# Kernel optimization log

Hardware: AMD Instinct MI355X
Metric: run time of the kernel (lower is better)

## Reference

```python
import jax, jax.numpy as jnp
import numpy as np

EPS = 1e-9

def _cheb_attention_conv(X_real, X_imag, lap_real, lap_imag,
                         Wa_real, Wa_imag, ba_real, ba_imag,
                         modrelu_b, W_real, W_imag):
    B, N, C = X_real.shape
    # --- attention scores: CVLinear over cat([x_i, x_j]) == (X@W1)_i + (X@W2)_j + b ---
    W1r, W2r = Wa_real[:C, 0], Wa_real[C:, 0]  # [C]
    W1i, W2i = Wa_imag[:C, 0], Wa_imag[C:, 0]
    # complex matvec: (Xr + iXi)(Wr + iWi)
    si_r = X_real @ W1r - X_imag @ W1i          # [B,N] contribution of x_i
    si_i = X_real @ W1i + X_imag @ W1r
    sj_r = X_real @ W2r - X_imag @ W2i          # [B,N] contribution of x_j
    sj_i = X_real @ W2i + X_imag @ W2r
    sc_r = si_r[:, :, None] + sj_r[:, None, :] + ba_real[0]   # [B,N,N]
    sc_i = si_i[:, :, None] + sj_i[:, None, :] + ba_imag[0]
    # --- learnable modReLU: relu(|z| + b) * z/|z| ---
    mag = jnp.sqrt(sc_r * sc_r + sc_i * sc_i)
    scale = jax.nn.relu(mag + modrelu_b[0]) / (mag + EPS)
    sc_r = sc_r * scale
    sc_i = sc_i * scale
    # --- split complex softmax over last dim ---
    a_r = jax.nn.softmax(sc_r, axis=-1)
    a_i = jax.nn.softmax(sc_i, axis=-1)
    # --- reweight Laplacian polynomials (complex mult, broadcast over k) ---
    L_r = lap_real * a_r[:, None] - lap_imag * a_i[:, None]   # [B,K+1,N,N]
    L_i = lap_real * a_i[:, None] + lap_imag * a_r[:, None]
    # --- sum_k (L_k X) W_k, complex ---
    LX_r = jnp.einsum('bkij,bjc->bkic', L_r, X_real) - jnp.einsum('bkij,bjc->bkic', L_i, X_imag)
    LX_i = jnp.einsum('bkij,bjc->bkic', L_r, X_imag) + jnp.einsum('bkij,bjc->bkic', L_i, X_real)
    out_r = jnp.einsum('bkic,kco->bio', LX_r, W_real) - jnp.einsum('bkic,kco->bio', LX_i, W_imag)
    out_i = jnp.einsum('bkic,kco->bio', LX_r, W_imag) + jnp.einsum('bkic,kco->bio', LX_i, W_real)
    return out_r, out_i


def setup_inputs() -> dict:
    key = jax.random.key(0)
    ks = jax.random.split(key, 8)
    B, N, C, CO, K1 = 48, 512, 64, 64, 5
    # weights normalized to unit complex magnitude like the torch init
    wr = jax.random.uniform(ks[4], (K1, C, CO), minval=-1.0, maxval=1.0) / np.sqrt(CO)
    wi = jax.random.uniform(ks[5], (K1, C, CO), minval=-1.0, maxval=1.0) / np.sqrt(CO)
    m = jnp.sqrt(wr * wr + wi * wi)
    return {
        'X_real': jax.random.normal(ks[0], (B, N, C), jnp.float32),
        'X_imag': jax.random.normal(ks[1], (B, N, C), jnp.float32),
        'lap_real': jax.random.normal(ks[2], (B, K1, N, N), jnp.float32) * 0.1,
        'lap_imag': jax.random.normal(ks[3], (B, K1, N, N), jnp.float32) * 0.1,
        'Wa_real': jax.random.normal(ks[6], (2 * C, 1), jnp.float32) * 0.1,
        'Wa_imag': jax.random.normal(ks[7], (2 * C, 1), jnp.float32) * 0.1,
        'ba_real': jnp.zeros((1,), jnp.float32),
        'ba_imag': jnp.zeros((1,), jnp.float32),
        'modrelu_b': jnp.zeros((1,), jnp.float32),
        'W_real': (wr / m).astype(jnp.float32),
        'W_imag': (wi / m).astype(jnp.float32),
    }


def reference(X_real, X_imag, lap_real, lap_imag, Wa_real, Wa_imag,
              ba_real, ba_imag, modrelu_b, W_real, W_imag):
    out_r, out_i = _cheb_attention_conv(X_real, X_imag, lap_real, lap_imag,
                                        Wa_real, Wa_imag, ba_real, ba_imag,
                                        modrelu_b, W_real, W_imag)
    return out_r, out_i
```

## Files before the change

kernel.cpp:

```cpp
#include <hip/hip_runtime.h>

#define EPSF 1e-9f

typedef __attribute__((ext_vector_type(8))) short short8;
typedef __attribute__((ext_vector_type(4))) float f32x4;
typedef __attribute__((ext_vector_type(4))) unsigned int u32x4;
typedef __attribute__((ext_vector_type(2))) unsigned int u32x2;

__device__ __forceinline__ unsigned pkbf(float lo, float hi) {
  unsigned r;
  asm("v_cvt_pk_bf16_f32 %0, %1, %2" : "=v"(r) : "v"(lo), "v"(hi));
  return r;
}
__device__ __forceinline__ short8 mk8(unsigned a, unsigned b, unsigned c, unsigned d) {
  u32x4 u = {a, b, c, d};
  return __builtin_bit_cast(short8, u);
}

__global__ __launch_bounds__(256) void k_s(
    const float* __restrict__ Xr, const float* __restrict__ Xi,
    const float* __restrict__ War, const float* __restrict__ Wai,
    float4* __restrict__ s4, float2* __restrict__ sj2)
{
  int t = threadIdx.x;
  int nf = blockIdx.x * 32 + (t >> 3);
  int c0 = (t & 7) * 8;
  const f32x4* xr = (const f32x4*)(Xr + (size_t)nf * 64 + c0);
  const f32x4* xi = (const f32x4*)(Xi + (size_t)nf * 64 + c0);
  const f32x4* w1r = (const f32x4*)(War + c0);
  const f32x4* w2r = (const f32x4*)(War + 64 + c0);
  const f32x4* w1i = (const f32x4*)(Wai + c0);
  const f32x4* w2i = (const f32x4*)(Wai + 64 + c0);
  float sir = 0.f, sii = 0.f, sjr = 0.f, sji = 0.f;
#pragma unroll
  for (int h = 0; h < 2; ++h) {
    f32x4 a = xr[h], bb = xi[h];
    f32x4 u1r = w1r[h], u1i = w1i[h], u2r = w2r[h], u2i = w2i[h];
#pragma unroll
    for (int e = 0; e < 4; ++e) {
      sir += a[e] * u1r[e] - bb[e] * u1i[e];
      sii += a[e] * u1i[e] + bb[e] * u1r[e];
      sjr += a[e] * u2r[e] - bb[e] * u2i[e];
      sji += a[e] * u2i[e] + bb[e] * u2r[e];
    }
  }
#pragma unroll
  for (int off = 1; off < 8; off <<= 1) {
    sir += __shfl_xor(sir, off);
    sii += __shfl_xor(sii, off);
    sjr += __shfl_xor(sjr, off);
    sji += __shfl_xor(sji, off);
  }
  if ((t & 7) == 0) {
    s4[nf] = make_float4(sir, sii, sjr, sji);
    sj2[nf] = make_float2(sjr, sji);
  }
}

__global__ __launch_bounds__(256) void k_stats(
    const float4* __restrict__ s4, const float2* __restrict__ sj2,
    const float* __restrict__ bar, const float* __restrict__ bai,
    const float* __restrict__ modbp, float4* __restrict__ stats)
{
  __shared__ float2 sh[512];
  int t = threadIdx.x;
  int b = blockIdx.x >> 4;
  int i0 = (blockIdx.x & 15) * 32;
  sh[t] = sj2[(size_t)b * 512 + t];
  sh[t + 256] = sj2[(size_t)b * 512 + t + 256];
  __syncthreads();
  float ba_r = bar[0], ba_i = bai[0], modb = modbp[0];
  int i = i0 + (t >> 3), jl = t & 7;
  float4 sv = s4[(size_t)b * 512 + i];
  float sirb = sv.x + ba_r, siib = sv.y + ba_i;
  float mr = -1e30f, mi = -1e30f;
  for (int jj = 0; jj < 64; ++jj) {
    float2 sj = sh[jl * 64 + jj];
    float scr = sirb + sj.x, sci = siib + sj.y;
    float mag = sqrtf(scr * scr + sci * sci);
    float sc = fmaxf(mag + modb, 0.f) * __builtin_amdgcn_rcpf(mag + EPSF);
    mr = fmaxf(mr, scr * sc);
    mi = fmaxf(mi, sci * sc);
  }
#pragma unroll
  for (int off = 1; off < 8; off <<= 1) {
    mr = fmaxf(mr, __shfl_xor(mr, off));
    mi = fmaxf(mi, __shfl_xor(mi, off));
  }
  float er = 0.f, ei = 0.f;
  for (int jj = 0; jj < 64; ++jj) {
    float2 sj = sh[jl * 64 + jj];
    float scr = sirb + sj.x, sci = siib + sj.y;
    float mag = sqrtf(scr * scr + sci * sci);
    float sc = fmaxf(mag + modb, 0.f) * __builtin_amdgcn_rcpf(mag + EPSF);
    er += __expf(scr * sc - mr);
    ei += __expf(sci * sc - mi);
  }
#pragma unroll
  for (int off = 1; off < 8; off <<= 1) {
    er += __shfl_xor(er, off);
    ei += __shfl_xor(ei, off);
  }
  if (jl == 0)
    stats[(size_t)b * 512 + i] = make_float4(mr, 1.f / er, mi, 1.f / ei);
}

__global__ __launch_bounds__(256) void k_y(
    const float* __restrict__ Xr, const float* __restrict__ Xi,
    const float* __restrict__ Wr, const float* __restrict__ Wi,
    u32x4* __restrict__ yfrag)
{
  __shared__ __align__(16) short WtR[64 * 72];
  __shared__ __align__(16) short WtI[64 * 72];
  __shared__ __align__(16) short Yt[4][2][64 * 24];
  int bk = blockIdx.x;
  int b = bk / 5, k = bk % 5;
  int t = threadIdx.x;
  {
    int o = t & 63, cbase = (t >> 6) * 16;
    const float* wr = Wr + (size_t)k * 4096;
    const float* wi = Wi + (size_t)k * 4096;
#pragma unroll
    for (int cc = 0; cc < 16; cc += 2) {
      int c = cbase + cc;
      *(unsigned*)&WtR[o * 72 + c] = pkbf(wr[c * 64 + o], wr[(c + 1) * 64 + o]);
      *(unsigned*)&WtI[o * 72 + c] = pkbf(wi[c * 64 + o], wi[(c + 1) * 64 + o]);
    }
  }
  __syncthreads();
  int w = t >> 6, l = t & 63;
  int lane15 = l & 15, quad = l >> 4;
  short* ytR = &Yt[w][0][0];
  short* ytI = &Yt[w][1][0];
  for (int qq = 0; qq < 8; ++qq) {
    int q = w * 8 + qq;
    int j = q * 16 + lane15;
    const f32x4* pxr = (const f32x4*)(Xr + ((size_t)b * 512 + j) * 64 + quad * 8);
    const f32x4* pxi = (const f32x4*)(Xi + ((size_t)b * 512 + j) * 64 + quad * 8);
    f32x4 xr0 = pxr[0], xr1 = pxr[1], xr8 = pxr[8], xr9 = pxr[9];
    f32x4 xi0 = pxi[0], xi1 = pxi[1], xi8 = pxi[8], xi9 = pxi[9];
    short8 axr[2], axi[2];
    axr[0] = mk8(pkbf(xr0[0], xr0[1]), pkbf(xr0[2], xr0[3]), pkbf(xr1[0], xr1[1]), pkbf(xr1[2], xr1[3]));
    axr[1] = mk8(pkbf(xr8[0], xr8[1]), pkbf(xr8[2], xr8[3]), pkbf(xr9[0], xr9[1]), pkbf(xr9[2], xr9[3]));
    axi[0] = mk8(pkbf(xi0[0], xi0[1]), pkbf(xi0[2], xi0[3]), pkbf(xi1[0], xi1[1]), pkbf(xi1[2], xi1[3]));
    axi[1] = mk8(pkbf(xi8[0], xi8[1]), pkbf(xi8[2], xi8[3]), pkbf(xi9[0], xi9[1]), pkbf(xi9[2], xi9[3]));
    f32x4 aR1[4], aR2[4], aI[4];
#pragma unroll
    for (int os = 0; os < 4; ++os) {
      aR1[os] = f32x4{0.f, 0.f, 0.f, 0.f};
      aR2[os] = f32x4{0.f, 0.f, 0.f, 0.f};
      aI[os] = f32x4{0.f, 0.f, 0.f, 0.f};
    }
#pragma unroll
    for (int kc = 0; kc < 2; ++kc) {
#pragma unroll
      for (int os = 0; os < 4; ++os) {
        int widx = (os * 16 + lane15) * 72 + kc * 32 + quad * 8;
        short8 wrF = *(const short8*)&WtR[widx];
        short8 wiF = *(const short8*)&WtI[widx];
        aR1[os] = __builtin_amdgcn_mfma_f32_16x16x32_bf16(axr[kc], wrF, aR1[os], 0, 0, 0);
        aR2[os] = __builtin_amdgcn_mfma_f32_16x16x32_bf16(axi[kc], wiF, aR2[os], 0, 0, 0);
        aI[os]  = __builtin_amdgcn_mfma_f32_16x16x32_bf16(axr[kc], wiF, aI[os], 0, 0, 0);
        aI[os]  = __builtin_amdgcn_mfma_f32_16x16x32_bf16(axi[kc], wrF, aI[os], 0, 0, 0);
      }
    }
#pragma unroll
    for (int os = 0; os < 4; ++os) {
      f32x4 R = aR1[os] - aR2[os];
      f32x4 I = aI[os];
      int ya = (os * 16 + lane15) * 24 + quad * 4;
      *(u32x2*)&ytR[ya] = u32x2{pkbf(R[0], R[1]), pkbf(R[2], R[3])};
      *(u32x2*)&ytI[ya] = u32x2{pkbf(I[0], I[1]), pkbf(I[2], I[3])};
    }
#pragma unroll
    for (int part = 0; part < 2; ++part) {
      const short* yt = part ? ytI : ytR;
#pragma unroll
      for (int h = 0; h < 2; ++h) {
        short8 unit = *(const short8*)&yt[l * 24 + h * 8];
        size_t line = (((size_t)(b * 5 + k) * 2 + part) * 16 + (q >> 1)) * 4 + (l >> 4);
        size_t idx = line * 64 + ((q & 1) * 2 + h) * 16 + (l & 15);
        yfrag[idx] = __builtin_bit_cast(u32x4, unit);
      }
    }
  }
}

__global__ __launch_bounds__(256) __attribute__((amdgpu_waves_per_eu(2, 2)))
void k_main(
    const float* __restrict__ lapr, const float* __restrict__ lapi,
    const float4* __restrict__ s4, const float4* __restrict__ stats,
    const float2* __restrict__ sj2, const u32x4* __restrict__ yfrag,
    const float* __restrict__ bar, const float* __restrict__ bai,
    const float* __restrict__ modbp,
    float* __restrict__ out_r, float* __restrict__ out_i)
{
  __shared__ __align__(16) f32x4 red[2][64][8];

  const int g = blockIdx.x;
  const int b = (g & 7) + ((g >> 8) << 3);
  const int it = (g >> 3) & 31;
  const int t = threadIdx.x;
  const int w = t >> 6;
  const int l = t & 63;
  const int lane15 = l & 15, quad = l >> 4;
  const int gi = it * 16 + lane15;

  float ba_r = bar[0], ba_i = bai[0], modb = modbp[0];
  float4 sv = s4[(size_t)b * 512 + gi];
  float4 st = stats[(size_t)b * 512 + gi];
  float sirb = sv.x + ba_r, siib = sv.y + ba_i;
  float maxr = st.x, rsr = st.y, maxi = st.z, rsi = st.w;

  f32x4 accR[4], accI[4];
#pragma unroll
  for (int os = 0; os < 4; ++os) {
    accR[os] = f32x4{0.f, 0.f, 0.f, 0.f};
    accI[os] = f32x4{0.f, 0.f, 0.f, 0.f};
  }

  const size_t NN = (size_t)512 * 512;
  const float* lapr_b = lapr + ((size_t)b * 5 * 512 + gi) * 512;
  const float* lapi_b = lapi + ((size_t)b * 5 * 512 + gi) * 512;
  const u32x4* yb = yfrag + (size_t)b * 5 * 8192 + l;

  for (int jsw = 0; jsw < 4; ++jsw) {
    const int js = w * 4 + jsw;
    const int jq = js * 32 + quad * 8;

    const f32x4* sjp = (const f32x4*)(sj2 + (size_t)b * 512 + jq);
    f32x4 sjv0 = sjp[0], sjv1 = sjp[1], sjv2 = sjp[2], sjv3 = sjp[3];

    f32x4 LR[5][2], LI[5][2];
#pragma unroll
    for (int k = 0; k < 5; ++k) {
      const f32x4* pr = (const f32x4*)(lapr_b + (size_t)k * NN + jq);
      const f32x4* pi_ = (const f32x4*)(lapi_b + (size_t)k * NN + jq);
      LR[k][0] = __builtin_nontemporal_load(pr);
      LR[k][1] = __builtin_nontemporal_load(pr + 1);
      LI[k][0] = __builtin_nontemporal_load(pi_);
      LI[k][1] = __builtin_nontemporal_load(pi_ + 1);
    }
    __builtin_amdgcn_sched_barrier(0);

    float sjr[8] = {sjv0[0], sjv0[2], sjv1[0], sjv1[2], sjv2[0], sjv2[2], sjv3[0], sjv3[2]};
    float sjimag[8] = {sjv0[1], sjv0[3], sjv1[1], sjv1[3], sjv2[1], sjv2[3], sjv3[1], sjv3[3]};
    float ar[8], ai[8];
#pragma unroll
    for (int e = 0; e < 8; ++e) {
      float scr = sirb + sjr[e];
      float sci = siib + sjimag[e];
      float mag = __builtin_amdgcn_sqrtf(fmaf(scr, scr, sci * sci));
      float sc = fmaxf(mag + modb, 0.f) * __builtin_amdgcn_rcpf(mag + EPSF);
      ar[e] = __expf(fmaf(scr, sc, -maxr)) * rsr;
      ai[e] = __expf(fmaf(sci, sc, -maxi)) * rsi;
    }

#pragma unroll
    for (int k = 0; k < 5; ++k) {
      float lrv[8], liv[8];
#pragma unroll
      for (int e = 0; e < 4; ++e) {
        lrv[e]     = LR[k][0][e] * ar[e]     - LI[k][0][e] * ai[e];
        liv[e]     = LR[k][0][e] * ai[e]     + LI[k][0][e] * ar[e];
        lrv[4 + e] = LR[k][1][e] * ar[4 + e] - LI[k][1][e] * ai[4 + e];
        liv[4 + e] = LR[k][1][e] * ai[4 + e] + LI[k][1][e] * ar[4 + e];
      }
      unsigned p0 = pkbf(lrv[0], lrv[1]), p1 = pkbf(lrv[2], lrv[3]);
      unsigned p2 = pkbf(lrv[4], lrv[5]), p3 = pkbf(lrv[6], lrv[7]);
      unsigned q0 = pkbf(liv[0], liv[1]), q1 = pkbf(liv[2], liv[3]);
      unsigned q2 = pkbf(liv[4], liv[5]), q3 = pkbf(liv[6], liv[7]);
      short8 Ar = mk8(p0, p1, p2, p3);
      short8 Ai = mk8(q0, q1, q2, q3);
      short8 An = mk8(q0 ^ 0x80008000u, q1 ^ 0x80008000u,
                      q2 ^ 0x80008000u, q3 ^ 0x80008000u);

      const u32x4* yk = yb + (size_t)k * 8192 + (size_t)(js * 4) * 64;
#pragma unroll
      for (int os = 0; os < 4; ++os) {
        short8 br8 = __builtin_bit_cast(short8, yk[os * 64]);
        short8 bi8 = __builtin_bit_cast(short8, yk[4096 + os * 64]);
        accR[os] = __builtin_amdgcn_mfma_f32_16x16x32_bf16(Ar, br8, accR[os], 0, 0, 0);
        accR[os] = __builtin_amdgcn_mfma_f32_16x16x32_bf16(An, bi8, accR[os], 0, 0, 0);
        accI[os] = __builtin_amdgcn_mfma_f32_16x16x32_bf16(Ar, bi8, accI[os], 0, 0, 0);
        accI[os] = __builtin_amdgcn_mfma_f32_16x16x32_bf16(Ai, br8, accI[os], 0, 0, 0);
      }
    }
  }

  if (w >= 2) {
#pragma unroll
    for (int os = 0; os < 4; ++os) {
      red[w - 2][l][os] = accR[os];
      red[w - 2][l][4 + os] = accI[os];
    }
  }
  __syncthreads();
  if (w < 2) {
#pragma unroll
    for (int os = 0; os < 4; ++os) {
      accR[os] += red[w][l][os];
      accI[os] += red[w][l][4 + os];
    }
  }
  __syncthreads();
  if (w == 1) {
#pragma unroll
    for (int os = 0; os < 4; ++os) {
      red[0][l][os] = accR[os];
      red[0][l][4 + os] = accI[os];
    }
  }
  __syncthreads();
  if (w == 0) {
#pragma unroll
    for (int os = 0; os < 4; ++os) {
      accR[os] += red[0][l][os];
      accI[os] += red[0][l][4 + os];
      int oc = os * 16 + lane15;
#pragma unroll
      for (int r = 0; r < 4; ++r) {
        size_t oidx = ((size_t)b * 512 + it * 16 + quad * 4 + r) * 64 + oc;
        out_r[oidx] = accR[os][r];
        out_i[oidx] = accI[os][r];
      }
    }
  }
}

extern "C" void kernel_launch(void* const* d_in, const int* in_sizes, int n_in,
                              void* d_out, int out_size, void* d_ws, size_t ws_size,
                              hipStream_t stream) {
  const float* Xr = (const float*)d_in[0];
  const float* Xi = (const float*)d_in[1];
  const float* lapr = (const float*)d_in[2];
  const float* lapi = (const float*)d_in[3];
  const float* War = (const float*)d_in[4];
  const float* Wai = (const float*)d_in[5];
  const float* bar = (const float*)d_in[6];
  const float* bai = (const float*)d_in[7];
  const float* modb = (const float*)d_in[8];
  const float* Wr = (const float*)d_in[9];
  const float* Wi = (const float*)d_in[10];

  char* wsb = (char*)d_ws;
  float4* s4 = (float4*)wsb;
  float4* stats = (float4*)(wsb + 393216);
  float2* sj2 = (float2*)(wsb + 786432);
  u32x4* yfrag = (u32x4*)(wsb + 983040);

  float* out_r = (float*)d_out;
  float* out_i = out_r + (size_t)48 * 512 * 64;

  k_s<<<768, 256, 0, stream>>>(Xr, Xi, War, Wai, s4, sj2);
  k_stats<<<768, 256, 0, stream>>>(s4, sj2, bar, bai, modb, stats);
  k_y<<<240, 256, 0, stream>>>(Xr, Xi, Wr, Wi, yfrag);
  k_main<<<1536, 256, 0, stream>>>(lapr, lapi, s4, stats, sj2, yfrag,
                                   bar, bai, modb, out_r, out_i);
}
```

Measured before the change: 190.8 us.

## Split k_main into single-wave blocks with partial outputs and separate reduction kernel

```diff
diff --git a/kernel.cpp b/kernel.cpp
--- a/kernel.cpp
+++ b/kernel.cpp
@@ -113,7 +113,8 @@
   __shared__ __align__(16) short WtR[64 * 72];
   __shared__ __align__(16) short WtI[64 * 72];
   __shared__ __align__(16) short Yt[4][2][64 * 24];
-  int bk = blockIdx.x;
+  int bk = blockIdx.x >> 2;
+  int jh = blockIdx.x & 3;
   int b = bk / 5, k = bk % 5;
   int t = threadIdx.x;
   {
@@ -132,8 +133,8 @@
   int lane15 = l & 15, quad = l >> 4;
   short* ytR = &Yt[w][0][0];
   short* ytI = &Yt[w][1][0];
-  for (int qq = 0; qq < 8; ++qq) {
-    int q = w * 8 + qq;
+  for (int qq = 0; qq < 2; ++qq) {
+    int q = jh * 8 + w * 2 + qq;
     int j = q * 16 + lane15;
     const f32x4* pxr = (const f32x4*)(Xr + ((size_t)b * 512 + j) * 64 + quad * 8);
     const f32x4* pxi = (const f32x4*)(Xi + ((size_t)b * 512 + j) * 64 + quad * 8);
@@ -186,23 +187,23 @@
   }
 }
 
-__global__ __launch_bounds__(256) __attribute__((amdgpu_waves_per_eu(2, 2)))
+__global__ __launch_bounds__(64) __attribute__((amdgpu_waves_per_eu(4, 4)))
 void k_main(
     const float* __restrict__ lapr, const float* __restrict__ lapi,
     const float4* __restrict__ s4, const float4* __restrict__ stats,
     const float2* __restrict__ sj2, const u32x4* __restrict__ yfrag,
     const float* __restrict__ bar, const float* __restrict__ bai,
     const float* __restrict__ modbp,
-    float* __restrict__ out_r, float* __restrict__ out_i)
-{
-  __shared__ __align__(16) f32x4 red[2][64][8];
-
+    float* __restrict__ partR, float* __restrict__ partI)
+{
   const int g = blockIdx.x;
-  const int b = (g & 7) + ((g >> 8) << 3);
-  const int it = (g >> 3) & 31;
-  const int t = threadIdx.x;
-  const int w = t >> 6;
-  const int l = t & 63;
+  const int bl = g & 7;
+  const int g2 = g >> 3;
+  const int it = g2 & 31;
+  const int sl = (g2 >> 5) & 3;
+  const int bh = g2 >> 7;
+  const int b = bl + (bh << 3);
+  const int l = threadIdx.x;
   const int lane15 = l & 15, quad = l >> 4;
   const int gi = it * 16 + lane15;
 
@@ -225,7 +226,7 @@
   const u32x4* yb = yfrag + (size_t)b * 5 * 8192 + l;
 
   for (int jsw = 0; jsw < 4; ++jsw) {
-    const int js = w * 4 + jsw;
+    const int js = sl * 4 + jsw;
     const int jq = js * 32 + quad * 8;
 
     const f32x4* sjp = (const f32x4*)(sj2 + (size_t)b * 512 + jq);
@@ -288,44 +289,29 @@
     }
   }
 
-  if (w >= 2) {
-#pragma unroll
-    for (int os = 0; os < 4; ++os) {
-      red[w - 2][l][os] = accR[os];
-      red[w - 2][l][4 + os] = accI[os];
-    }
-  }
-  __syncthreads();
-  if (w < 2) {
-#pragma unroll
-    for (int os = 0; os < 4; ++os) {
-      accR[os] += red[w][l][os];
-      accI[os] += red[w][l][4 + os];
-    }
-  }
-  __syncthreads();
-  if (w == 1) {
-#pragma unroll
-    for (int os = 0; os < 4; ++os) {
-      red[0][l][os] = accR[os];
-      red[0][l][4 + os] = accI[os];
-    }
-  }
-  __syncthreads();
-  if (w == 0) {
-#pragma unroll
-    for (int os = 0; os < 4; ++os) {
-      accR[os] += red[0][l][os];
-      accI[os] += red[0][l][4 + os];
-      int oc = os * 16 + lane15;
-#pragma unroll
-      for (int r = 0; r < 4; ++r) {
-        size_t oidx = ((size_t)b * 512 + it * 16 + quad * 4 + r) * 64 + oc;
-        out_r[oidx] = accR[os][r];
-        out_i[oidx] = accI[os][r];
-      }
-    }
-  }
+  const size_t pbase = ((size_t)sl * 48 + b) * 512;
+#pragma unroll
+  for (int os = 0; os < 4; ++os) {
+    int oc = os * 16 + lane15;
+#pragma unroll
+    for (int r = 0; r < 4; ++r) {
+      size_t oidx = (pbase + it * 16 + quad * 4 + r) * 64 + oc;
+      partR[oidx] = accR[os][r];
+      partI[oidx] = accI[os][r];
+    }
+  }
+}
+
+__global__ __launch_bounds__(256) void k_red(
+    const f32x4* __restrict__ partR, const f32x4* __restrict__ partI,
+    f32x4* __restrict__ out_r, f32x4* __restrict__ out_i)
+{
+  const size_t NPART = (size_t)48 * 512 * 64 / 4;
+  size_t x = (size_t)blockIdx.x * 256 + threadIdx.x;
+  f32x4 r = partR[x] + partR[NPART + x] + partR[2 * NPART + x] + partR[3 * NPART + x];
+  f32x4 i = partI[x] + partI[NPART + x] + partI[2 * NPART + x] + partI[3 * NPART + x];
+  out_r[x] = r;
+  out_i[x] = i;
 }
 
 extern "C" void kernel_launch(void* const* d_in, const int* in_sizes, int n_in,
@@ -348,13 +334,17 @@
   float4* stats = (float4*)(wsb + 393216);
   float2* sj2 = (float2*)(wsb + 786432);
   u32x4* yfrag = (u32x4*)(wsb + 983040);
+  float* partR = (float*)(wsb + 983040 + 31457280);
+  float* partI = partR + (size_t)4 * 48 * 512 * 64;
 
   float* out_r = (float*)d_out;
   float* out_i = out_r + (size_t)48 * 512 * 64;
 
   k_s<<<768, 256, 0, stream>>>(Xr, Xi, War, Wai, s4, sj2);
   k_stats<<<768, 256, 0, stream>>>(s4, sj2, bar, bai, modb, stats);
-  k_y<<<240, 256, 0, stream>>>(Xr, Xi, Wr, Wi, yfrag);
-  k_main<<<1536, 256, 0, stream>>>(lapr, lapi, s4, stats, sj2, yfrag,
-                                   bar, bai, modb, out_r, out_i);
-}
+  k_y<<<960, 256, 0, stream>>>(Xr, Xi, Wr, Wi, yfrag);
+  k_main<<<6144, 64, 0, stream>>>(lapr, lapi, s4, stats, sj2, yfrag,
+                                  bar, bai, modb, partR, partI);
+  k_red<<<1536, 256, 0, stream>>>((const f32x4*)partR, (const f32x4*)partI,
+                                  (f32x4*)out_r, (f32x4*)out_i);
+}
```

Result: slower. 293.3 us (+53.7%).
